# Kernel optimization log

Measured on AMD Instinct MI355X. Metric: run time of the kernel, lower is better.

## Reference

```python
import jax, jax.numpy as jnp
import numpy as np

BATCH = 128
L = 4096
DIM = 64
N = 3   # rate-1/3 encoder: three 1-channel branches concatenated
EPS = 1e-3  # keras BatchNormalization default epsilon


def _bn(y, g, be, m, v):
    # inference-mode BatchNormalization over the channel (last) axis
    return g * (y - m) * jax.lax.rsqrt(v + EPS) + be


def _circ_unit(x, w, b, g, be, m, v):
    # Circular 'same' padding for kernel_size=5, stride=1 -> pad_window = 2
    xp = jnp.concatenate([x[:, -2:], x, x[:, :2]], axis=1)  # [B, L+4, C]
    y = jax.lax.conv_general_dilated(
        xp, w, window_strides=(1,), padding='VALID',
        dimension_numbers=('NWC', 'WIO', 'NWC')) + b        # [B, L, DIM]
    return jax.nn.elu(_bn(y, g, be, m, v))


def setup_inputs() -> dict:
    key = jax.random.key(0)
    ks = iter(jax.random.split(key, 16))

    def nrm(shape, s=0.05):
        return jax.random.normal(next(ks), shape, dtype=jnp.float32) * s

    inp = {}
    inp['x'] = jax.random.uniform(next(ks), (BATCH, L, 1), dtype=jnp.float32)
    # Pseudo_random_Interleaver: per-row permutation seeded by row index
    inp['perm'] = jnp.asarray(
        np.stack([np.random.RandomState(i).permutation(L) for i in range(BATCH)]),
        dtype=jnp.int32)
    for p in ('c1', 'c2', 'cI'):
        inp[p + '_w'] = nrm((5, 1, DIM)); inp[p + '_b'] = jnp.zeros((DIM,), jnp.float32)
        inp[p + '_g'] = jnp.ones((DIM,), jnp.float32); inp[p + '_be'] = jnp.zeros((DIM,), jnp.float32)
        inp[p + '_m'] = jnp.zeros((DIM,), jnp.float32); inp[p + '_v'] = jnp.ones((DIM,), jnp.float32)
    for p in ('f1', 'f2', 'fI'):
        inp[p + '_w'] = nrm((DIM, 1)); inp[p + '_b'] = jnp.zeros((1,), jnp.float32)
    inp['mp_w'] = nrm((1, DIM)); inp['mp_b'] = jnp.zeros((DIM,), jnp.float32)
    inp['mp_g'] = jnp.ones((DIM,), jnp.float32); inp['mp_be'] = jnp.zeros((DIM,), jnp.float32)
    inp['mp_m'] = jnp.zeros((DIM,), jnp.float32); inp['mp_v'] = jnp.ones((DIM,), jnp.float32)
    inp['md_w'] = nrm((DIM, 2)); inp['md_b'] = jnp.zeros((2,), jnp.float32)
    inp['md_g'] = jnp.ones((2,), jnp.float32); inp['md_be'] = jnp.zeros((2,), jnp.float32)
    inp['md_m'] = jnp.zeros((2,), jnp.float32); inp['md_v'] = jnp.ones((2,), jnp.float32)
    return inp


def reference(x, perm,
              c1_w, c1_b, c1_g, c1_be, c1_m, c1_v,
              c2_w, c2_b, c2_g, c2_be, c2_m, c2_v,
              cI_w, cI_b, cI_g, cI_be, cI_m, cI_v,
              f1_w, f1_b, f2_w, f2_b, fI_w, fI_b,
              mp_w, mp_b, mp_g, mp_be, mp_m, mp_v,
              md_w, md_b, md_g, md_be, md_m, md_v):
    x = 2.0 * x - 1.0  # bits -> +/-1
    # systematic branches
    e1 = jnp.einsum('bld,do->blo', _circ_unit(x, c1_w, c1_b, c1_g, c1_be, c1_m, c1_v), f1_w) + f1_b
    e2 = jnp.einsum('bld,do->blo', _circ_unit(x, c2_w, c2_b, c2_g, c2_be, c2_m, c2_v), f2_w) + f2_b
    # interleaved branch: one batched gather replaces the per-sample python loop
    xI = jnp.take_along_axis(x, perm[:, :, None], axis=1)
    eI = jnp.einsum('bld,do->blo', _circ_unit(xI, cI_w, cI_b, cI_g, cI_be, cI_m, cI_v), fI_w) + fI_b
    y = jnp.concatenate([e1, e2, eI], axis=-1)          # [B, L, 3]
    yt = y.reshape(BATCH, L * N, 1)                     # k = 1
    # Modulation: 1x1 conv (elu) then 1x1 conv to 2 coords (linear), each with BN
    mo = jax.nn.elu(_bn(jnp.einsum('blk,kd->bld', yt, mp_w) + mp_b, mp_g, mp_be, mp_m, mp_v))
    coord = _bn(jnp.einsum('bld,dc->blc', mo, md_w) + md_b, md_g, md_be, md_m, md_v)
    return coord  # [B, 3L, 2]
```

## Files before the change

### kernel.cpp

```cpp
#include <hip/hip_runtime.h>
#include <math.h>

#define BATCH 128
#define LL    4096
#define DIM   64
#define EPS   1e-3f
#define LUTN  2048

#define LOG2E 1.44269504088896340736f
#define LN2   0.69314718055994530942f

#define GC2 0.2402265069591007f
#define GC3 0.05550410866482158f
#define GC4 0.009618129107628477f
#define GC5 0.0013333558146428443f
#define GC6 1.540353039338161e-4f
#define GC7 1.525273380405984e-5f


typedef float f32x2 __attribute__((ext_vector_type(2)));

__device__ __forceinline__ f32x2 pk_fma(f32x2 a, f32x2 b, f32x2 c) {
    return __builtin_elementwise_fma(a, b, c);
}

__device__ __forceinline__ float elu_plain(float z) {
    return z > 0.0f ? z : (__expf(z) - 1.0f);
}

__global__ __launch_bounds__(256) void enc_prep(
    const float* __restrict__ cw0, const float* __restrict__ cb0, const float* __restrict__ cg0,
    const float* __restrict__ cbe0, const float* __restrict__ cm0, const float* __restrict__ cv0,
    const float* __restrict__ cw1, const float* __restrict__ cb1, const float* __restrict__ cg1,
    const float* __restrict__ cbe1, const float* __restrict__ cm1, const float* __restrict__ cv1,
    const float* __restrict__ cw2, const float* __restrict__ cb2, const float* __restrict__ cg2,
    const float* __restrict__ cbe2, const float* __restrict__ cm2, const float* __restrict__ cv2,
    const float* __restrict__ f0w, const float* __restrict__ f0b,
    const float* __restrict__ f1w, const float* __restrict__ f1b,
    const float* __restrict__ f2w, const float* __restrict__ f2b,
    const float* __restrict__ mpw, const float* __restrict__ mpb, const float* __restrict__ mpg,
    const float* __restrict__ mpbe, const float* __restrict__ mpm, const float* __restrict__ mpv,
    const float* __restrict__ mdw, const float* __restrict__ mdb, const float* __restrict__ mdg,
    const float* __restrict__ mdbe, const float* __restrict__ mdm, const float* __restrict__ mdv,
    float* __restrict__ W)
{
    const int t   = threadIdx.x;
    const int blk = blockIdx.x;
    __shared__ float smod[64][4];
    __shared__ float s_lo[3], s_hi[3];
    __shared__ float sD[2];
    __shared__ float srange[2];

    if (t < 192) {
        const int br = t >> 6;
        const int d  = t & 63;
        const float* cw  = (br == 0) ? cw0  : (br == 1) ? cw1  : cw2;
        const float* cb  = (br == 0) ? cb0  : (br == 1) ? cb1  : cb2;
        const float* cg  = (br == 0) ? cg0  : (br == 1) ? cg1  : cg2;
        const float* cbe = (br == 0) ? cbe0 : (br == 1) ? cbe1 : cbe2;
        const float* cm  = (br == 0) ? cm0  : (br == 1) ? cm1  : cm2;
        const float* cv  = (br == 0) ? cv0  : (br == 1) ? cv1  : cv2;
        const float* fw  = (br == 0) ? f0w  : (br == 1) ? f1w  : f2w;
        const float s = cg[d] / sqrtf(cv[d] + EPS);
        float tap[5], habs = 0.0f;
        #pragma unroll
        for (int k = 0; k < 5; ++k) {
            tap[k] = cw[k * 64 + d] * s * LOG2E;
            habs += fabsf(tap[k]);
        }
        const float bias = ((cb[d] - cm[d]) * s + cbe[d]) * LOG2E;
        const float fwd  = fw[d];
        if (blk == 0) {
            float* o = W + ((d >> 1) * 3 + br) * 16 + (d & 1);
            o[0] = tap[0]; o[2] = tap[1]; o[4] = tap[2]; o[6] = tap[3]; o[8] = tap[4];
            o[10] = bias; o[12] = fwd; o[14] = fwd * LN2;
        }
        const float hb = LN2 * (habs + fabsf(bias));
        float myS = fabsf(fwd) * fmaxf(1.0f, hb);
        #pragma unroll
        for (int off = 32; off; off >>= 1) {
            myS += __shfl_down(myS, off);
        }
        if ((t & 63) == 0) {
            const float fb = ((br == 0) ? f0b : (br == 1) ? f1b : f2b)[0];
            s_lo[br] = fb - myS;
            s_hi[br] = fb + myS;
            if (blk == 0) W[1792 + br] = fb;
        }
    } else {
        const int d = t - 192;
        const float smp = mpg[d] / sqrtf(mpv[d] + EPS);
        const float A = mpw[d] * smp;
        const float C = (mpb[d] - mpm[d]) * smp + mpbe[d];
        const float s0 = mdg[0] / sqrtf(mdv[0] + EPS);
        const float s1 = mdg[1] / sqrtf(mdv[1] + EPS);
        smod[d][0] = A;
        smod[d][1] = C;
        smod[d][2] = mdw[d * 2 + 0] * s0;
        smod[d][3] = mdw[d * 2 + 1] * s1;
        if (d == 0) {
            const float D0 = (mdb[0] - mdm[0]) * s0 + mdbe[0];
            const float D1 = (mdb[1] - mdm[1]) * s1 + mdbe[1];
            sD[0] = D0; sD[1] = D1;
            if (blk == 0) { W[1795] = D0; W[1796] = D1; }
        }
    }
    __syncthreads();

    if (t == 0) {
        float lo = fminf(s_lo[0], fminf(s_lo[1], s_lo[2]));
        float hi = fmaxf(s_hi[0], fmaxf(s_hi[1], s_hi[2]));
        float pad = 1e-3f * (hi - lo) + 1e-6f;
        lo -= pad; hi += pad;
        srange[0] = lo;
        srange[1] = (hi - lo) / (float)(LUTN - 1);
        if (blk == 0) {
            const float invh = (float)(LUTN - 1) / (hi - lo);
            W[1797] = invh;
            W[1798] = -lo * invh;
            W[1799] = lo;
        }
    }
    __syncthreads();

    const int i = blk * 256 + t;
    const float lo = srange[0], hs = srange[1];
    const float D0 = sD[0], D1 = sD[1];
    const float e0 = fmaf((float)i, hs, lo);
    const float e1 = fmaf((float)(i + 1), hs, lo);
    float a0 = D0, a1 = D1, b0 = D0, b1 = D1;
    #pragma unroll 8
    for (int d = 0; d < 64; ++d) {
        const float A = smod[d][0], C = smod[d][1], m0 = smod[d][2], m1 = smod[d][3];
        float u;
        u = elu_plain(fmaf(A, e0, C)); a0 = fmaf(m0, u, a0); a1 = fmaf(m1, u, a1);
        u = elu_plain(fmaf(A, e1, C)); b0 = fmaf(m0, u, b0); b1 = fmaf(m1, u, b1);
    }
    float4* lut = (float4*)(W + 1800);
    lut[i] = make_float4(a0, a1, b0 - a0, b1 - a1);
}

__device__ __forceinline__ float2 lut_eval(float e, float invh, float nlo,
                                           const float4* __restrict__ lut) {
    float tt = fminf(fmaxf(fmaf(e, invh, nlo), 0.0f), (float)(LUTN - 1));
    float fi = floorf(tt); float f = tt - fi;
    float4 v = lut[(int)fi];
    return make_float2(fmaf(f, v.z, v.x), fmaf(f, v.w, v.y));
}

__device__ __forceinline__ void elu_acc(f32x2 h, f32x2 fw, f32x2 fwl, f32x2& e,
                                        const f32x2 zero) {
    f32x2 z  = __builtin_elementwise_min(h, zero);
    f32x2 zz = z * z;
    f32x2 s  = pk_fma(z, f32x2{GC7, GC7}, f32x2{GC6, GC6});
    s = pk_fma(z, s, f32x2{GC5, GC5});
    s = pk_fma(z, s, f32x2{GC4, GC4});
    s = pk_fma(z, s, f32x2{GC3, GC3});
    s = pk_fma(z, s, f32x2{GC2, GC2});
    e = pk_fma(fw, zz * s, e);
    e = pk_fma(fwl, h, e);
}

__global__ __launch_bounds__(256) void enc_main(
    const float* __restrict__ x, const int* __restrict__ perm,
    const float* __restrict__ W, float* __restrict__ out)
{
    const int gid = blockIdx.x * 256 + threadIdx.x;
    const int b   = gid >> 11;
    const int l0  = (gid & (2048 - 1)) * 2;
    const float* xrow = x + ((size_t)b << 12);
    const int*   prow = perm + ((size_t)b << 12);

    int pidx[6];
    #pragma unroll
    for (int k = 0; k < 6; ++k) pidx[k] = prow[(l0 + k - 2) & (LL - 1)];
    float xw[6], xg[6];
    #pragma unroll
    for (int k = 0; k < 6; ++k) {
        xw[k] = fmaf(2.0f, xrow[(l0 + k - 2) & (LL - 1)], -1.0f);
        xg[k] = fmaf(2.0f, xrow[pidx[k]], -1.0f);
    }
    f32x2 xs[6], xi[6];
    #pragma unroll
    for (int k = 0; k < 6; ++k) {
        xs[k] = f32x2{xw[k], xw[k]};
        xi[k] = f32x2{xg[k], xg[k]};
    }

    f32x2 eA0 = {0.0f, 0.0f}, eA1 = {0.0f, 0.0f};
    f32x2 eB0 = {0.0f, 0.0f}, eB1 = {0.0f, 0.0f};
    f32x2 eC0 = {0.0f, 0.0f}, eC1 = {0.0f, 0.0f};
    const f32x2 zero = {0.0f, 0.0f};

    #pragma unroll 4
    for (int j = 0; j < 32; ++j) {
        const f32x2* tp = (const f32x2*)W + j * 24;
        f32x2 h;

        h = pk_fma(tp[0], xs[0], pk_fma(tp[1], xs[1], pk_fma(tp[2], xs[2],
            pk_fma(tp[3], xs[3], pk_fma(tp[4], xs[4], tp[5])))));
        elu_acc(h, tp[6], tp[7], eA0, zero);
        h = pk_fma(tp[0], xs[1], pk_fma(tp[1], xs[2], pk_fma(tp[2], xs[3],
            pk_fma(tp[3], xs[4], pk_fma(tp[4], xs[5], tp[5])))));
        elu_acc(h, tp[6], tp[7], eA1, zero);

        h = pk_fma(tp[8], xs[0], pk_fma(tp[9], xs[1], pk_fma(tp[10], xs[2],
            pk_fma(tp[11], xs[3], pk_fma(tp[12], xs[4], tp[13])))));
        elu_acc(h, tp[14], tp[15], eB0, zero);
        h = pk_fma(tp[8], xs[1], pk_fma(tp[9], xs[2], pk_fma(tp[10], xs[3],
            pk_fma(tp[11], xs[4], pk_fma(tp[12], xs[5], tp[13])))));
        elu_acc(h, tp[14], tp[15], eB1, zero);

        h = pk_fma(tp[16], xi[0], pk_fma(tp[17], xi[1], pk_fma(tp[18], xi[2],
            pk_fma(tp[19], xi[3], pk_fma(tp[20], xi[4], tp[21])))));
        elu_acc(h, tp[22], tp[23], eC0, zero);
        h = pk_fma(tp[16], xi[1], pk_fma(tp[17], xi[2], pk_fma(tp[18], xi[3],
            pk_fma(tp[19], xi[4], pk_fma(tp[20], xi[5], tp[21])))));
        elu_acc(h, tp[22], tp[23], eC1, zero);
    }

    const float fbA = W[1792], fbB = W[1793], fbC = W[1794];
    const float sA0 = fbA + eA0.x + eA0.y, sA1 = fbA + eA1.x + eA1.y;
    const float sB0 = fbB + eB0.x + eB0.y, sB1 = fbB + eB1.x + eB1.y;
    const float sC0 = fbC + eC0.x + eC0.y, sC1 = fbC + eC1.x + eC1.y;

    const float invh = W[1797], nlo = W[1798];
    const float4* lut = (const float4*)(W + 1800);
    float2 r0 = lut_eval(sA0, invh, nlo, lut);
    float2 r1 = lut_eval(sB0, invh, nlo, lut);
    float2 r2 = lut_eval(sC0, invh, nlo, lut);
    float2 r3 = lut_eval(sA1, invh, nlo, lut);
    float2 r4 = lut_eval(sB1, invh, nlo, lut);
    float2 r5 = lut_eval(sC1, invh, nlo, lut);

    float4* o4 = (float4*)(out + (size_t)gid * 12);
    o4[0] = make_float4(r0.x, r0.y, r1.x, r1.y);
    o4[1] = make_float4(r2.x, r2.y, r3.x, r3.y);
    o4[2] = make_float4(r4.x, r4.y, r5.x, r5.y);
}

extern "C" void kernel_launch(void* const* d_in, const int* in_sizes, int n_in,
                              void* d_out, int out_size, void* d_ws, size_t ws_size,
                              hipStream_t stream) {
    const float* x    = (const float*)d_in[0];
    const int*   perm = (const int*)d_in[1];
    float* W = (float*)d_ws;

    enc_prep<<<LUTN / 256, 256, 0, stream>>>(
        (const float*)d_in[2],  (const float*)d_in[3],  (const float*)d_in[4],
        (const float*)d_in[5],  (const float*)d_in[6],  (const float*)d_in[7],
        (const float*)d_in[8],  (const float*)d_in[9],  (const float*)d_in[10],
        (const float*)d_in[11], (const float*)d_in[12], (const float*)d_in[13],
        (const float*)d_in[14], (const float*)d_in[15], (const float*)d_in[16],
        (const float*)d_in[17], (const float*)d_in[18], (const float*)d_in[19],
        (const float*)d_in[20], (const float*)d_in[21],
        (const float*)d_in[22], (const float*)d_in[23],
        (const float*)d_in[24], (const float*)d_in[25],
        (const float*)d_in[26], (const float*)d_in[27], (const float*)d_in[28],
        (const float*)d_in[29], (const float*)d_in[30], (const float*)d_in[31],
        (const float*)d_in[32], (const float*)d_in[33], (const float*)d_in[34],
        (const float*)d_in[35], (const float*)d_in[36], (const float*)d_in[37],
        W);

    enc_main<<<(BATCH * LL) / 512, 256, 0, stream>>>(x, perm, W, (float*)d_out);
}
```

Before: 38.06 us.

## Hoist linear ELU term out of channel loop and shorten polynomial

The linear part of the ELU-times-projection sum (fw*h) is reduced across channels in the prep kernel into a 5-tap collapsed filter, so the main loop only accumulates the nonlinear correction. The polynomial used to approximate exp for negative inputs is cut from degree 7 to degree 5, and the x and perm window loads are vectorized into float2/int2 loads. Together these remove about a third of the per-iteration packed FMAs in the hot loop. The lower-degree polynomial adds approximation error for large negative pre-activations.

```diff
diff --git a/kernel.cpp b/kernel.cpp
--- a/kernel.cpp
+++ b/kernel.cpp
@@ -14,8 +14,6 @@
 #define GC3 0.05550410866482158f
 #define GC4 0.009618129107628477f
 #define GC5 0.0013333558146428443f
-#define GC6 1.540353039338161e-4f
-#define GC7 1.525273380405984e-5f
 
 
 typedef float f32x2 __attribute__((ext_vector_type(2)));
@@ -73,19 +71,32 @@
         if (blk == 0) {
             float* o = W + ((d >> 1) * 3 + br) * 16 + (d & 1);
             o[0] = tap[0]; o[2] = tap[1]; o[4] = tap[2]; o[6] = tap[3]; o[8] = tap[4];
-            o[10] = bias; o[12] = fwd; o[14] = fwd * LN2;
+            o[10] = bias; o[12] = fwd;
         }
         const float hb = LN2 * (habs + fabsf(bias));
+        float r0 = fwd * tap[0], r1 = fwd * tap[1], r2 = fwd * tap[2];
+        float r3 = fwd * tap[3], r4 = fwd * tap[4], rb = fwd * bias;
         float myS = fabsf(fwd) * fmaxf(1.0f, hb);
         #pragma unroll
         for (int off = 32; off; off >>= 1) {
+            r0 += __shfl_down(r0, off);
+            r1 += __shfl_down(r1, off);
+            r2 += __shfl_down(r2, off);
+            r3 += __shfl_down(r3, off);
+            r4 += __shfl_down(r4, off);
+            rb += __shfl_down(rb, off);
             myS += __shfl_down(myS, off);
         }
         if ((t & 63) == 0) {
             const float fb = ((br == 0) ? f0b : (br == 1) ? f1b : f2b)[0];
             s_lo[br] = fb - myS;
             s_hi[br] = fb + myS;
-            if (blk == 0) W[1792 + br] = fb;
+            if (blk == 0) {
+                float* Lb = W + 1536 + br * 8;
+                Lb[0] = LN2 * r0; Lb[1] = LN2 * r1; Lb[2] = LN2 * r2;
+                Lb[3] = LN2 * r3; Lb[4] = LN2 * r4; Lb[5] = LN2 * rb;
+                W[1560 + br] = fb;
+            }
         }
     } else {
         const int d = t - 192;
@@ -102,7 +113,7 @@
             const float D0 = (mdb[0] - mdm[0]) * s0 + mdbe[0];
             const float D1 = (mdb[1] - mdm[1]) * s1 + mdbe[1];
             sD[0] = D0; sD[1] = D1;
-            if (blk == 0) { W[1795] = D0; W[1796] = D1; }
+            if (blk == 0) { W[1563] = D0; W[1564] = D1; }
         }
     }
     __syncthreads();
@@ -116,9 +127,9 @@
         srange[1] = (hi - lo) / (float)(LUTN - 1);
         if (blk == 0) {
             const float invh = (float)(LUTN - 1) / (hi - lo);
-            W[1797] = invh;
-            W[1798] = -lo * invh;
-            W[1799] = lo;
+            W[1565] = invh;
+            W[1566] = -lo * invh;
+            W[1567] = lo;
         }
     }
     __syncthreads();
@@ -136,7 +147,7 @@
         u = elu_plain(fmaf(A, e0, C)); a0 = fmaf(m0, u, a0); a1 = fmaf(m1, u, a1);
         u = elu_plain(fmaf(A, e1, C)); b0 = fmaf(m0, u, b0); b1 = fmaf(m1, u, b1);
     }
-    float4* lut = (float4*)(W + 1800);
+    float4* lut = (float4*)(W + 1568);
     lut[i] = make_float4(a0, a1, b0 - a0, b1 - a1);
 }
 
@@ -148,17 +159,14 @@
     return make_float2(fmaf(f, v.z, v.x), fmaf(f, v.w, v.y));
 }
 
-__device__ __forceinline__ void elu_acc(f32x2 h, f32x2 fw, f32x2 fwl, f32x2& e,
-                                        const f32x2 zero) {
+__device__ __forceinline__ void nl_acc(f32x2 h, f32x2 fw, f32x2& e) {
+    const f32x2 zero = {0.0f, 0.0f};
     f32x2 z  = __builtin_elementwise_min(h, zero);
     f32x2 zz = z * z;
-    f32x2 s  = pk_fma(z, f32x2{GC7, GC7}, f32x2{GC6, GC6});
-    s = pk_fma(z, s, f32x2{GC5, GC5});
-    s = pk_fma(z, s, f32x2{GC4, GC4});
+    f32x2 s  = pk_fma(z, f32x2{GC5, GC5}, f32x2{GC4, GC4});
     s = pk_fma(z, s, f32x2{GC3, GC3});
     s = pk_fma(z, s, f32x2{GC2, GC2});
     e = pk_fma(fw, zz * s, e);
-    e = pk_fma(fwl, h, e);
 }
 
 __global__ __launch_bounds__(256) void enc_main(
@@ -171,15 +179,23 @@
     const float* xrow = x + ((size_t)b << 12);
     const int*   prow = perm + ((size_t)b << 12);
 
-    int pidx[6];
-    #pragma unroll
-    for (int k = 0; k < 6; ++k) pidx[k] = prow[(l0 + k - 2) & (LL - 1)];
+    const int ba = (l0 - 2) & (LL - 1);
+    const int bc = (l0 + 2) & (LL - 1);
+    const float2 w01 = *(const float2*)(xrow + ba);
+    const float2 w23 = *(const float2*)(xrow + l0);
+    const float2 w45 = *(const float2*)(xrow + bc);
+    const int2 p01 = *(const int2*)(prow + ba);
+    const int2 p23 = *(const int2*)(prow + l0);
+    const int2 p45 = *(const int2*)(prow + bc);
+
     float xw[6], xg[6];
-    #pragma unroll
-    for (int k = 0; k < 6; ++k) {
-        xw[k] = fmaf(2.0f, xrow[(l0 + k - 2) & (LL - 1)], -1.0f);
-        xg[k] = fmaf(2.0f, xrow[pidx[k]], -1.0f);
-    }
+    xw[0] = fmaf(2.0f, w01.x, -1.0f); xw[1] = fmaf(2.0f, w01.y, -1.0f);
+    xw[2] = fmaf(2.0f, w23.x, -1.0f); xw[3] = fmaf(2.0f, w23.y, -1.0f);
+    xw[4] = fmaf(2.0f, w45.x, -1.0f); xw[5] = fmaf(2.0f, w45.y, -1.0f);
+    xg[0] = fmaf(2.0f, xrow[p01.x], -1.0f); xg[1] = fmaf(2.0f, xrow[p01.y], -1.0f);
+    xg[2] = fmaf(2.0f, xrow[p23.x], -1.0f); xg[3] = fmaf(2.0f, xrow[p23.y], -1.0f);
+    xg[4] = fmaf(2.0f, xrow[p45.x], -1.0f); xg[5] = fmaf(2.0f, xrow[p45.y], -1.0f);
+
     f32x2 xs[6], xi[6];
     #pragma unroll
     for (int k = 0; k < 6; ++k) {
@@ -187,10 +203,25 @@
         xi[k] = f32x2{xg[k], xg[k]};
     }
 
+    const float* LA = W + 1536;
+    const float* LB = W + 1544;
+    const float* LC = W + 1552;
+    float linA0 = fmaf(LA[0], xw[0], fmaf(LA[1], xw[1], fmaf(LA[2], xw[2],
+                  fmaf(LA[3], xw[3], fmaf(LA[4], xw[4], LA[5])))));
+    float linA1 = fmaf(LA[0], xw[1], fmaf(LA[1], xw[2], fmaf(LA[2], xw[3],
+                  fmaf(LA[3], xw[4], fmaf(LA[4], xw[5], LA[5])))));
+    float linB0 = fmaf(LB[0], xw[0], fmaf(LB[1], xw[1], fmaf(LB[2], xw[2],
+                  fmaf(LB[3], xw[3], fmaf(LB[4], xw[4], LB[5])))));
+    float linB1 = fmaf(LB[0], xw[1], fmaf(LB[1], xw[2], fmaf(LB[2], xw[3],
+                  fmaf(LB[3], xw[4], fmaf(LB[4], xw[5], LB[5])))));
+    float linC0 = fmaf(LC[0], xg[0], fmaf(LC[1], xg[1], fmaf(LC[2], xg[2],
+                  fmaf(LC[3], xg[3], fmaf(LC[4], xg[4], LC[5])))));
+    float linC1 = fmaf(LC[0], xg[1], fmaf(LC[1], xg[2], fmaf(LC[2], xg[3],
+                  fmaf(LC[3], xg[4], fmaf(LC[4], xg[5], LC[5])))));
+
     f32x2 eA0 = {0.0f, 0.0f}, eA1 = {0.0f, 0.0f};
     f32x2 eB0 = {0.0f, 0.0f}, eB1 = {0.0f, 0.0f};
     f32x2 eC0 = {0.0f, 0.0f}, eC1 = {0.0f, 0.0f};
-    const f32x2 zero = {0.0f, 0.0f};
 
     #pragma unroll 4
     for (int j = 0; j < 32; ++j) {
@@ -199,33 +230,36 @@
 
         h = pk_fma(tp[0], xs[0], pk_fma(tp[1], xs[1], pk_fma(tp[2], xs[2],
             pk_fma(tp[3], xs[3], pk_fma(tp[4], xs[4], tp[5])))));
-        elu_acc(h, tp[6], tp[7], eA0, zero);
+        nl_acc(h, tp[6], eA0);
         h = pk_fma(tp[0], xs[1], pk_fma(tp[1], xs[2], pk_fma(tp[2], xs[3],
             pk_fma(tp[3], xs[4], pk_fma(tp[4], xs[5], tp[5])))));
-        elu_acc(h, tp[6], tp[7], eA1, zero);
+        nl_acc(h, tp[6], eA1);
 
         h = pk_fma(tp[8], xs[0], pk_fma(tp[9], xs[1], pk_fma(tp[10], xs[2],
             pk_fma(tp[11], xs[3], pk_fma(tp[12], xs[4], tp[13])))));
-        elu_acc(h, tp[14], tp[15], eB0, zero);
+        nl_acc(h, tp[14], eB0);
         h = pk_fma(tp[8], xs[1], pk_fma(tp[9], xs[2], pk_fma(tp[10], xs[3],
             pk_fma(tp[11], xs[4], pk_fma(tp[12], xs[5], tp[13])))));
-        elu_acc(h, tp[14], tp[15], eB1, zero);
+        nl_acc(h, tp[14], eB1);
 
         h = pk_fma(tp[16], xi[0], pk_fma(tp[17], xi[1], pk_fma(tp[18], xi[2],
             pk_fma(tp[19], xi[3], pk_fma(tp[20], xi[4], tp[21])))));
-        elu_acc(h, tp[22], tp[23], eC0, zero);
+        nl_acc(h, tp[22], eC0);
         h = pk_fma(tp[16], xi[1], pk_fma(tp[17], xi[2], pk_fma(tp[18], xi[3],
             pk_fma(tp[19], xi[4], pk_fma(tp[20], xi[5], tp[21])))));
-        elu_acc(h, tp[22], tp[23], eC1, zero);
-    }
-
-    const float fbA = W[1792], fbB = W[1793], fbC = W[1794];
-    const float sA0 = fbA + eA0.x + eA0.y, sA1 = fbA + eA1.x + eA1.y;
-    const float sB0 = fbB + eB0.x + eB0.y, sB1 = fbB + eB1.x + eB1.y;
-    const float sC0 = fbC + eC0.x + eC0.y, sC1 = fbC + eC1.x + eC1.y;
-
-    const float invh = W[1797], nlo = W[1798];
-    const float4* lut = (const float4*)(W + 1800);
+        nl_acc(h, tp[22], eC1);
+    }
+
+    const float fbA = W[1560], fbB = W[1561], fbC = W[1562];
+    const float sA0 = fbA + linA0 + eA0.x + eA0.y;
+    const float sA1 = fbA + linA1 + eA1.x + eA1.y;
+    const float sB0 = fbB + linB0 + eB0.x + eB0.y;
+    const float sB1 = fbB + linB1 + eB1.x + eB1.y;
+    const float sC0 = fbC + linC0 + eC0.x + eC0.y;
+    const float sC1 = fbC + linC1 + eC1.x + eC1.y;
+
+    const float invh = W[1565], nlo = W[1566];
+    const float4* lut = (const float4*)(W + 1568);
     float2 r0 = lut_eval(sA0, invh, nlo, lut);
     float2 r1 = lut_eval(sB0, invh, nlo, lut);
     float2 r2 = lut_eval(sC0, invh, nlo, lut);
```

Result: faster. 35.69 us (-6.2%).
